# Kernel optimization log

Measured on AMD Instinct MI355X. Metric: run time of the kernel, lower is better.

## Reference

```python
import jax, jax.numpy as jnp
import numpy as np
from functools import partial


def advect(f, vx, vy):
    """Semi-Lagrangian advection with bilinear interpolation and periodic wrap.
    Faithful to the torch version, including its xy-indexed meshgrid."""
    rows, cols = f.shape
    # torch.meshgrid(arange(rows), arange(cols), indexing='xy') == np.meshgrid semantics
    cell_ys, cell_xs = jnp.meshgrid(jnp.arange(rows), jnp.arange(cols), indexing='xy')
    center_xs = (cell_xs - vx).ravel()
    center_ys = (cell_ys - vy).ravel()
    left_ix = jnp.floor(center_xs).astype(jnp.int32)
    top_ix = jnp.floor(center_ys).astype(jnp.int32)
    rw = center_xs - left_ix  # right weight
    bw = center_ys - top_ix   # bottom weight
    left_ix = jnp.mod(left_ix, rows)
    right_ix = jnp.mod(left_ix + 1, rows)
    top_ix = jnp.mod(top_ix, cols)
    bot_ix = jnp.mod(top_ix + 1, cols)
    flat_f = ((1 - rw) * ((1 - bw) * f[left_ix, top_ix] + bw * f[left_ix, bot_ix])
              + rw * ((1 - bw) * f[right_ix, top_ix] + bw * f[right_ix, bot_ix]))
    return flat_f.reshape(rows, cols)


def project(vx, vy):
    """Approximate pressure projection: 10 Jacobi iterations of a 5-point stencil."""
    h = 1.0 / vx.shape[0]
    div = -0.5 * h * (jnp.roll(vx, -1, axis=0) - jnp.roll(vx, 1, axis=0)
                      + jnp.roll(vy, -1, axis=1) - jnp.roll(vy, 1, axis=1))

    def jacobi(k, p):
        return (div + jnp.roll(p, 1, axis=0) + jnp.roll(p, -1, axis=0)
                + jnp.roll(p, 1, axis=1) + jnp.roll(p, -1, axis=1)) / 4.0

    p = jax.lax.fori_loop(0, 10, jacobi, jnp.zeros_like(vx))
    vx = vx - 0.5 * (jnp.roll(p, -1, axis=0) - jnp.roll(p, 1, axis=0)) / h
    vy = vy - 0.5 * (jnp.roll(p, -1, axis=1) - jnp.roll(p, 1, axis=1)) / h
    return vx, vy


def simulate(vx, vy, smoke, num_time_steps):
    def step(carry, _):
        vx, vy, smoke = carry
        vx_upd = advect(vx, vx, vy)
        vy_upd = advect(vy, vx, vy)
        vx, vy = project(vx_upd, vy_upd)
        smoke = advect(smoke, vx, vy)
        return (vx, vy, smoke), None

    (vx, vy, smoke), _ = jax.lax.scan(step, (vx, vy, smoke), None, length=num_time_steps)
    return smoke


def setup_inputs() -> dict:
    key = jax.random.key(0)
    k1, k2, k3 = jax.random.split(key, 3)
    N = 2048
    smoke = jax.random.uniform(k1, (N, N), dtype=jnp.float32)
    init_vx = jax.random.normal(k2, (N, N), dtype=jnp.float32)
    init_vy = jax.random.normal(k3, (N, N), dtype=jnp.float32)
    return {"smoke": smoke, "init_vx": init_vx, "init_vy": init_vy,
            "num_time_steps": 20}


def reference(smoke, init_vx, init_vy, num_time_steps):
    return simulate(init_vx, init_vy, smoke, num_time_steps)
```

## Files before the change

### kernel.cpp

```cpp
#include <hip/hip_runtime.h>

namespace {

constexpr int N = 2048;
constexpr int MASK = N - 1;
constexpr int SH = 11;
constexpr float H = 1.0f / (float)N;

using f32x2 = __attribute__((ext_vector_type(2))) float;


__device__ __forceinline__ float dpp_left(float x) {
  return __int_as_float(__builtin_amdgcn_update_dpp(
      0, __float_as_int(x), 0x111 , 0xF, 0xF, true));
}
__device__ __forceinline__ float dpp_right(float x) {
  return __int_as_float(__builtin_amdgcn_update_dpp(
      0, __float_as_int(x), 0x101 , 0xF, 0xF, true));
}

__global__ __launch_bounds__(256) void advect_vel_k(
    const float* __restrict__ vx, const float* __restrict__ vy,
    float2* __restrict__ OV) {
  int bid = blockIdx.x;
  int sb = ((bid & 7) << 11) | (bid >> 3);
  int idx = sb * 256 + threadIdx.x;
  int i = idx >> SH, j = idx & MASK;
  float cx = (float)i - vx[idx];
  float cy = (float)j - vy[idx];
  float fx = floorf(cx), fy = floorf(cy);
  float rw = cx - fx, bw = cy - fy;
  int l = ((int)fx) & MASK;
  int t = ((int)fy) & MASK;
  int r = (l + 1) & MASK;
  int b = (t + 1) & MASK;
  int i00 = (l << SH) | t, i01 = (l << SH) | b;
  int i10 = (r << SH) | t, i11 = (r << SH) | b;
  float omr = 1.0f - rw, omb = 1.0f - bw;
  float w00 = omr * omb, w01 = omr * bw, w10 = rw * omb, w11 = rw * bw;
  float2 o;
  o.x = w00 * vx[i00] + w01 * vx[i01] + w10 * vx[i10] + w11 * vx[i11];
  o.y = w00 * vy[i00] + w01 * vy[i01] + w10 * vy[i10] + w11 * vy[i11];
  OV[idx] = o;
}

__global__ __launch_bounds__(256) void advect_all_k(
    const float* __restrict__ f,
    const float2* __restrict__ V,
    float* __restrict__ of, float2* __restrict__ OV) {
  int bid = blockIdx.x;
  int sb = ((bid & 7) << 10) | (bid >> 3);
  int t0 = sb * 256 + threadIdx.x;
  int j  = t0 & MASK;
  int i0 = (t0 >> SH) * 2;
  int idx0 = (i0 << SH) | j;
  int idx1 = idx0 + N;

  float2 v0 = V[idx0];
  float2 v1 = V[idx1];

  float cx0 = (float)i0 - v0.x, cy0 = (float)j - v0.y;
  float fx0 = floorf(cx0), fy0 = floorf(cy0);
  float rw0 = cx0 - fx0, bw0 = cy0 - fy0;
  int l0 = ((int)fx0) & MASK, tt0 = ((int)fy0) & MASK;
  int r0 = (l0 + 1) & MASK,  b0 = (tt0 + 1) & MASK;
  int a00 = (l0 << SH) | tt0, a01 = (l0 << SH) | b0;
  int a10 = (r0 << SH) | tt0, a11 = (r0 << SH) | b0;

  float cx1 = (float)(i0 + 1) - v1.x, cy1 = (float)j - v1.y;
  float fx1 = floorf(cx1), fy1 = floorf(cy1);
  float rw1 = cx1 - fx1, bw1 = cy1 - fy1;
  int l1 = ((int)fx1) & MASK, tt1 = ((int)fy1) & MASK;
  int r1 = (l1 + 1) & MASK,  b1 = (tt1 + 1) & MASK;
  int c00 = (l1 << SH) | tt1, c01 = (l1 << SH) | b1;
  int c10 = (r1 << SH) | tt1, c11 = (r1 << SH) | b1;

  float2 g00a = V[a00], g01a = V[a01], g10a = V[a10], g11a = V[a11];
  float  f00a = f[a00], f01a = f[a01], f10a = f[a10], f11a = f[a11];
  float2 g00c = V[c00], g01c = V[c01], g10c = V[c10], g11c = V[c11];
  float  f00c = f[c00], f01c = f[c01], f10c = f[c10], f11c = f[c11];

  float omr0 = 1.0f - rw0, omb0 = 1.0f - bw0;
  float w00a = omr0 * omb0, w01a = omr0 * bw0, w10a = rw0 * omb0, w11a = rw0 * bw0;
  float omr1 = 1.0f - rw1, omb1 = 1.0f - bw1;
  float w00c = omr1 * omb1, w01c = omr1 * bw1, w10c = rw1 * omb1, w11c = rw1 * bw1;

  of[idx0] = w00a * f00a + w01a * f01a + w10a * f10a + w11a * f11a;
  float2 o0;
  o0.x = w00a * g00a.x + w01a * g01a.x + w10a * g10a.x + w11a * g11a.x;
  o0.y = w00a * g00a.y + w01a * g01a.y + w10a * g10a.y + w11a * g11a.y;
  OV[idx0] = o0;
  of[idx1] = w00c * f00c + w01c * f01c + w10c * f10c + w11c * f11c;
  float2 o1;
  o1.x = w00c * g00c.x + w01c * g01c.x + w10c * g10c.x + w11c * g11c.x;
  o1.y = w00c * g00c.y + w01c * g01c.y + w10c * g10c.y + w11c * g11c.y;
  OV[idx1] = o1;
}

__global__ __launch_bounds__(256) void advect_smoke_k(
    const float* __restrict__ f,
    const float2* __restrict__ V,
    float* __restrict__ of) {
  int bid = blockIdx.x;
  int sb = ((bid & 7) << 11) | (bid >> 3);
  int idx = sb * 256 + threadIdx.x;
  int i = idx >> SH, j = idx & MASK;
  float2 v = V[idx];
  float cx = (float)i - v.x;
  float cy = (float)j - v.y;
  float fx = floorf(cx), fy = floorf(cy);
  float rw = cx - fx, bw = cy - fy;
  int l = ((int)fx) & MASK;
  int t = ((int)fy) & MASK;
  int r = (l + 1) & MASK;
  int b = (t + 1) & MASK;
  float f00 = f[(l << SH) | t];
  float f01 = f[(l << SH) | b];
  float f10 = f[(r << SH) | t];
  float f11 = f[(r << SH) | b];
  float omr = 1.0f - rw, omb = 1.0f - bw;
  of[idx] = omr * (omb * f00 + bw * f01) + rw * (omb * f10 + bw * f11);
}

__device__ __forceinline__ float4 jac_row(float4 dd, float4 vu, float4 vd, float4 o) {
  float pl = dpp_left(o.w);
  float pr = dpp_right(o.x);
  f32x2 dlo = {dd.x, dd.y}, dhi = {dd.z, dd.w};
  f32x2 vulo = {vu.x, vu.y}, vuhi = {vu.z, vu.w};
  f32x2 vdlo = {vd.x, vd.y}, vdhi = {vd.z, vd.w};
  f32x2 lft = {pl, o.x};
  f32x2 mid = {o.y, o.z};
  f32x2 rgt = {o.w, pr};
  f32x2 lo = (dlo + vulo + vdlo + lft + mid) * 0.25f;
  f32x2 hi = (dhi + vuhi + vdhi + mid + rgt) * 0.25f;
  return float4{lo.x, lo.y, hi.x, hi.y};
}

__device__ __forceinline__ void div_p1(float4 au, float4 ad, float4 b,
                                       float4& dq, float4& pq) {
  float yl = dpp_left(b.w);
  float yr = dpp_right(b.x);
  constexpr float s = -0.5f * H;
  f32x2 vlo = f32x2{ad.x, ad.y} - f32x2{au.x, au.y};
  f32x2 vhi = f32x2{ad.z, ad.w} - f32x2{au.z, au.w};
  f32x2 hlo = f32x2{b.y, b.z} - f32x2{yl, b.x};
  f32x2 hhi = f32x2{b.w, yr} - f32x2{b.y, b.z};
  f32x2 dlo = (vlo + hlo) * s;
  f32x2 dhi = (vhi + hhi) * s;
  f32x2 plo = dlo * 0.25f;
  f32x2 phi = dhi * 0.25f;
  dq = float4{dlo.x, dlo.y, dhi.x, dhi.y};
  pq = float4{plo.x, plo.y, phi.x, phi.y};
}

__global__ __launch_bounds__(512, 6) void project_k(
    const float2* __restrict__ V,
    float2* __restrict__ OV) {
  __shared__ __align__(16) float pA[90 * 64];
  __shared__ __align__(16) float pB[90 * 64];

  const int tid = threadIdx.x;
  const int bid = blockIdx.x;
  const int sbid = ((bid & 7) << 8) | (bid >> 3);
  const int tile_i = sbid >> 6;
  const int tile_j = sbid & 63;
  const int bi = tile_i * 64 - 11;
  const int cj0 = tile_j * 32 - 16;

  for (int e = tid; e < 86 * 32; e += 512) {
    int row = e >> 5;
    int u = e & 31;
    int gi = (bi + row) & MASK;
    int gj = (cj0 + u * 2) & MASK;
    int gg = (gi << SH) | gj;
    float4 q = *(const float4*)&V[gg];
    *(float2*)&pA[(row + 1) * 64 + u * 2] = float2{q.x, q.z};
    *(float2*)&pB[(row + 1) * 64 + u * 2] = float2{q.y, q.w};
  }
  __syncthreads();

  const int g = tid >> 4;
  const int c0 = (tid & 15) * 4;
  const bool act = (g < 29);
  const int r0 = 3 * g;
  float4 p[3], d[3];
#pragma unroll
  for (int q = 0; q < 3; ++q) { p[q] = float4{0,0,0,0}; d[q] = float4{0,0,0,0}; }

  if (act) {
    const int lb = r0 * 64 + c0;
    float4 a0 = *(const float4*)&pA[lb];
    float4 a1 = *(const float4*)&pA[lb + 64];
    float4 a2 = *(const float4*)&pA[lb + 128];
    float4 a3 = *(const float4*)&pA[lb + 192];
    float4 a4 = *(const float4*)&pA[lb + 256];
    float4 b0 = *(const float4*)&pB[lb + 64];
    float4 b1 = *(const float4*)&pB[lb + 128];
    float4 b2 = *(const float4*)&pB[lb + 192];
    div_p1(a0, a2, b0, d[0], p[0]);
    div_p1(a1, a3, b1, d[1], p[1]);
    div_p1(a2, a4, b2, d[2], p[2]);
  }
  __syncthreads();

#pragma unroll
  for (int k = 0; k < 9; ++k) {
    float* w = (k & 1) ? pB : pA;
    if (act) {
      *(float4*)&w[(r0 + 1) * 64 + c0] = p[0];
      *(float4*)&w[(r0 + 3) * 64 + c0] = p[2];
    }
    __syncthreads();
    if (act) {
      float4 up = *(const float4*)&w[(r0 + 0) * 64 + c0];
      float4 dn = *(const float4*)&w[(r0 + 4) * 64 + c0];
      float4 o0 = p[0], o1 = p[1];
      p[0] = jac_row(d[0], up, o1, o0);
      p[1] = jac_row(d[1], o0, p[2], o1);
      p[2] = jac_row(d[2], o1, dn, p[2]);
    }
  }

  if (act) {
    *(float4*)&pB[(r0 + 1) * 64 + c0] = p[0];
    *(float4*)&pB[(r0 + 2) * 64 + c0] = p[1];
    *(float4*)&pB[(r0 + 3) * 64 + c0] = p[2];
  }
  __syncthreads();

  const float c = 0.5f / H;
#pragma unroll
  for (int q = 0; q < 4; ++q) {
    int pth = tid + q * 512;
    int oi = pth >> 5, oj = pth & 31;
    int gi = tile_i * 64 + oi;
    int gj = tile_j * 32 + oj;
    int gg = (gi << SH) | gj;
    float2 vc = V[gg];
    float2 o;
    o.x = vc.x - c * (pB[(13 + oi) * 64 + 16 + oj] - pB[(11 + oi) * 64 + 16 + oj]);
    o.y = vc.y - c * (pB[(12 + oi) * 64 + 17 + oj] - pB[(12 + oi) * 64 + 15 + oj]);
    OV[gg] = o;
  }
}

}

extern "C" void kernel_launch(void* const* d_in, const int* in_sizes, int n_in,
                              void* d_out, int out_size, void* d_ws, size_t ws_size,
                              hipStream_t stream) {
  const float* smoke_in = (const float*)d_in[0];
  const float* vx_in    = (const float*)d_in[1];
  const float* vy_in    = (const float*)d_in[2];
  float* out = (float*)d_out;

  const size_t fsz = (size_t)N * N;
  float* base = (float*)d_ws;
  float2* VC = (float2*)base;
  float2* VA = (float2*)(base + 2 * fsz);
  float*  SA = base + 4 * fsz;

  dim3 ablk(256), agrd((N * N) / 256);
  dim3 a2grd((N * N) / 512);
  dim3 pblk(512), pgrd(32 * 64);
  const int steps = 20;

  const float* ssrc = smoke_in;

  advect_vel_k<<<agrd, ablk, 0, stream>>>(vx_in, vy_in, VC);

  for (int t = 0; t < steps; ++t) {
    project_k<<<pgrd, pblk, 0, stream>>>(VC, VA);
    float* sdst = (t & 1) ? out : SA;
    if (t < steps - 1) {
      advect_all_k<<<a2grd, ablk, 0, stream>>>(ssrc, VA, sdst, VC);
    } else {
      advect_smoke_k<<<agrd, ablk, 0, stream>>>(ssrc, VA, sdst);
    }
    ssrc = sdst;
  }
}
```

Measured before the change: 1.017 ms.

## Pack velocity and smoke into interleaved float4 so gathers use one load

```diff
diff --git a/kernel.cpp b/kernel.cpp
--- a/kernel.cpp
+++ b/kernel.cpp
@@ -44,10 +44,20 @@
   OV[idx] = o;
 }
 
-__global__ __launch_bounds__(256) void advect_all_k(
-    const float* __restrict__ f,
-    const float2* __restrict__ V,
-    float* __restrict__ of, float2* __restrict__ OV) {
+__global__ __launch_bounds__(256) void pack_smoke_k(
+    const float* __restrict__ f, float* __restrict__ Pf) {
+  int t = blockIdx.x * 256 + threadIdx.x;
+  float4 s = *(const float4*)&f[t * 4];
+  Pf[(t * 4 + 0) * 4 + 2] = s.x;
+  Pf[(t * 4 + 1) * 4 + 2] = s.y;
+  Pf[(t * 4 + 2) * 4 + 2] = s.z;
+  Pf[(t * 4 + 3) * 4 + 2] = s.w;
+}
+
+__global__ __launch_bounds__(256) void advect_packed_k(
+    const float4* __restrict__ P,
+    float* __restrict__ Pn,
+    float2* __restrict__ V2) {
   int bid = blockIdx.x;
   int sb = ((bid & 7) << 10) | (bid >> 3);
   int t0 = sb * 256 + threadIdx.x;
@@ -56,8 +66,9 @@
   int idx0 = (i0 << SH) | j;
   int idx1 = idx0 + N;
 
-  float2 v0 = V[idx0];
-  float2 v1 = V[idx1];
+  const float* Pf = (const float*)P;
+  float2 v0 = *(const float2*)&Pf[idx0 * 4];
+  float2 v1 = *(const float2*)&Pf[idx1 * 4];
 
   float cx0 = (float)i0 - v0.x, cy0 = (float)j - v0.y;
   float fx0 = floorf(cx0), fy0 = floorf(cy0);
@@ -75,16 +86,100 @@
   int c00 = (l1 << SH) | tt1, c01 = (l1 << SH) | b1;
   int c10 = (r1 << SH) | tt1, c11 = (r1 << SH) | b1;
 
+  float4 g00a = P[a00], g01a = P[a01], g10a = P[a10], g11a = P[a11];
+  float4 g00c = P[c00], g01c = P[c01], g10c = P[c10], g11c = P[c11];
+
+  float omr0 = 1.0f - rw0, omb0 = 1.0f - bw0;
+  float w00a = omr0 * omb0, w01a = omr0 * bw0, w10a = rw0 * omb0, w11a = rw0 * bw0;
+  float omr1 = 1.0f - rw1, omb1 = 1.0f - bw1;
+  float w00c = omr1 * omb1, w01c = omr1 * bw1, w10c = rw1 * omb1, w11c = rw1 * bw1;
+
+  float2 o0, o1;
+  o0.x = w00a * g00a.x + w01a * g01a.x + w10a * g10a.x + w11a * g11a.x;
+  o0.y = w00a * g00a.y + w01a * g01a.y + w10a * g10a.y + w11a * g11a.y;
+  float sm0 = w00a * g00a.z + w01a * g01a.z + w10a * g10a.z + w11a * g11a.z;
+  o1.x = w00c * g00c.x + w01c * g01c.x + w10c * g10c.x + w11c * g11c.x;
+  o1.y = w00c * g00c.y + w01c * g01c.y + w10c * g10c.y + w11c * g11c.y;
+  float sm1 = w00c * g00c.z + w01c * g01c.z + w10c * g10c.z + w11c * g11c.z;
+
+  V2[idx0] = o0;
+  V2[idx1] = o1;
+  Pn[idx0 * 4 + 2] = sm0;
+  Pn[idx1 * 4 + 2] = sm1;
+}
+
+__global__ __launch_bounds__(256) void advect_last_k(
+    const float4* __restrict__ P,
+    float* __restrict__ of) {
+  int bid = blockIdx.x;
+  int sb = ((bid & 7) << 10) | (bid >> 3);
+  int t0 = sb * 256 + threadIdx.x;
+  int j  = t0 & MASK;
+  int i0 = (t0 >> SH) * 2;
+  int idx0 = (i0 << SH) | j;
+  int idx1 = idx0 + N;
+
+  const float* Pf = (const float*)P;
+  float2 v0 = *(const float2*)&Pf[idx0 * 4];
+  float2 v1 = *(const float2*)&Pf[idx1 * 4];
+
+  float cx0 = (float)i0 - v0.x, cy0 = (float)j - v0.y;
+  float fx0 = floorf(cx0), fy0 = floorf(cy0);
+  float rw0 = cx0 - fx0, bw0 = cy0 - fy0;
+  int l0 = ((int)fx0) & MASK, tt0 = ((int)fy0) & MASK;
+  int r0 = (l0 + 1) & MASK,  b0 = (tt0 + 1) & MASK;
+  float4 g00a = P[(l0 << SH) | tt0], g01a = P[(l0 << SH) | b0];
+  float4 g10a = P[(r0 << SH) | tt0], g11a = P[(r0 << SH) | b0];
+
+  float cx1 = (float)(i0 + 1) - v1.x, cy1 = (float)j - v1.y;
+  float fx1 = floorf(cx1), fy1 = floorf(cy1);
+  float rw1 = cx1 - fx1, bw1 = cy1 - fy1;
+  int l1 = ((int)fx1) & MASK, tt1 = ((int)fy1) & MASK;
+  int r1 = (l1 + 1) & MASK,  b1 = (tt1 + 1) & MASK;
+  float4 g00c = P[(l1 << SH) | tt1], g01c = P[(l1 << SH) | b1];
+  float4 g10c = P[(r1 << SH) | tt1], g11c = P[(r1 << SH) | b1];
+
+  float omr0 = 1.0f - rw0, omb0 = 1.0f - bw0;
+  float omr1 = 1.0f - rw1, omb1 = 1.0f - bw1;
+  of[idx0] = omr0 * (omb0 * g00a.z + bw0 * g01a.z) + rw0 * (omb0 * g10a.z + bw0 * g11a.z);
+  of[idx1] = omr1 * (omb1 * g00c.z + bw1 * g01c.z) + rw1 * (omb1 * g10c.z + bw1 * g11c.z);
+}
+
+__global__ __launch_bounds__(256) void advect_all_k(
+    const float* __restrict__ f,
+    const float2* __restrict__ V,
+    float* __restrict__ of, float2* __restrict__ OV) {
+  int bid = blockIdx.x;
+  int sb = ((bid & 7) << 10) | (bid >> 3);
+  int t0 = sb * 256 + threadIdx.x;
+  int j  = t0 & MASK;
+  int i0 = (t0 >> SH) * 2;
+  int idx0 = (i0 << SH) | j;
+  int idx1 = idx0 + N;
+  float2 v0 = V[idx0];
+  float2 v1 = V[idx1];
+  float cx0 = (float)i0 - v0.x, cy0 = (float)j - v0.y;
+  float fx0 = floorf(cx0), fy0 = floorf(cy0);
+  float rw0 = cx0 - fx0, bw0 = cy0 - fy0;
+  int l0 = ((int)fx0) & MASK, tt0 = ((int)fy0) & MASK;
+  int r0 = (l0 + 1) & MASK,  b0 = (tt0 + 1) & MASK;
+  int a00 = (l0 << SH) | tt0, a01 = (l0 << SH) | b0;
+  int a10 = (r0 << SH) | tt0, a11 = (r0 << SH) | b0;
+  float cx1 = (float)(i0 + 1) - v1.x, cy1 = (float)j - v1.y;
+  float fx1 = floorf(cx1), fy1 = floorf(cy1);
+  float rw1 = cx1 - fx1, bw1 = cy1 - fy1;
+  int l1 = ((int)fx1) & MASK, tt1 = ((int)fy1) & MASK;
+  int r1 = (l1 + 1) & MASK,  b1 = (tt1 + 1) & MASK;
+  int c00 = (l1 << SH) | tt1, c01 = (l1 << SH) | b1;
+  int c10 = (r1 << SH) | tt1, c11 = (r1 << SH) | b1;
   float2 g00a = V[a00], g01a = V[a01], g10a = V[a10], g11a = V[a11];
   float  f00a = f[a00], f01a = f[a01], f10a = f[a10], f11a = f[a11];
   float2 g00c = V[c00], g01c = V[c01], g10c = V[c10], g11c = V[c11];
   float  f00c = f[c00], f01c = f[c01], f10c = f[c10], f11c = f[c11];
-
   float omr0 = 1.0f - rw0, omb0 = 1.0f - bw0;
   float w00a = omr0 * omb0, w01a = omr0 * bw0, w10a = rw0 * omb0, w11a = rw0 * bw0;
   float omr1 = 1.0f - rw1, omb1 = 1.0f - bw1;
   float w00c = omr1 * omb1, w01c = omr1 * bw1, w10c = rw1 * omb1, w11c = rw1 * bw1;
-
   of[idx0] = w00a * f00a + w01a * f01a + w10a * f10a + w11a * f11a;
   float2 o0;
   o0.x = w00a * g00a.x + w01a * g01a.x + w10a * g10a.x + w11a * g11a.x;
@@ -153,9 +248,10 @@
   pq = float4{plo.x, plo.y, phi.x, phi.y};
 }
 
+template <int OSTR>
 __global__ __launch_bounds__(512, 6) void project_k(
     const float2* __restrict__ V,
-    float2* __restrict__ OV) {
+    float* __restrict__ OVf) {
   __shared__ __align__(16) float pA[90 * 64];
   __shared__ __align__(16) float pB[90 * 64];
 
@@ -240,7 +336,7 @@
     float2 o;
     o.x = vc.x - c * (pB[(13 + oi) * 64 + 16 + oj] - pB[(11 + oi) * 64 + 16 + oj]);
     o.y = vc.y - c * (pB[(12 + oi) * 64 + 17 + oj] - pB[(12 + oi) * 64 + 15 + oj]);
-    OV[gg] = o;
+    *(float2*)&OVf[(size_t)gg * OSTR] = o;
   }
 }
 
@@ -256,27 +352,46 @@
 
   const size_t fsz = (size_t)N * N;
   float* base = (float*)d_ws;
-  float2* VC = (float2*)base;
-  float2* VA = (float2*)(base + 2 * fsz);
-  float*  SA = base + 4 * fsz;
 
   dim3 ablk(256), agrd((N * N) / 256);
   dim3 a2grd((N * N) / 512);
   dim3 pblk(512), pgrd(32 * 64);
   const int steps = 20;
 
-  const float* ssrc = smoke_in;
-
-  advect_vel_k<<<agrd, ablk, 0, stream>>>(vx_in, vy_in, VC);
-
-  for (int t = 0; t < steps; ++t) {
-    project_k<<<pgrd, pblk, 0, stream>>>(VC, VA);
-    float* sdst = (t & 1) ? out : SA;
-    if (t < steps - 1) {
-      advect_all_k<<<a2grd, ablk, 0, stream>>>(ssrc, VA, sdst, VC);
-    } else {
-      advect_smoke_k<<<agrd, ablk, 0, stream>>>(ssrc, VA, sdst);
+  const size_t need = fsz * 10 * sizeof(float);
+
+  if (ws_size >= need) {
+    float4* P0 = (float4*)base;
+    float4* P1 = (float4*)(base + 4 * fsz);
+    float2* V2 = (float2*)(base + 8 * fsz);
+
+    advect_vel_k<<<agrd, ablk, 0, stream>>>(vx_in, vy_in, V2);
+    pack_smoke_k<<<(N * N) / 1024, ablk, 0, stream>>>(smoke_in, (float*)P0);
+
+    for (int t = 0; t < steps; ++t) {
+      float4* Pc = (t & 1) ? P1 : P0;
+      float4* Pn = (t & 1) ? P0 : P1;
+      project_k<4><<<pgrd, pblk, 0, stream>>>(V2, (float*)Pc);
+      if (t < steps - 1)
+        advect_packed_k<<<a2grd, ablk, 0, stream>>>(Pc, (float*)Pn, V2);
+      else
+        advect_last_k<<<a2grd, ablk, 0, stream>>>(Pc, out);
     }
-    ssrc = sdst;
-  }
-}
+  } else {
+    float2* VC = (float2*)base;
+    float2* VA = (float2*)(base + 2 * fsz);
+    float*  SA = base + 4 * fsz;
+
+    const float* ssrc = smoke_in;
+    advect_vel_k<<<agrd, ablk, 0, stream>>>(vx_in, vy_in, VC);
+    for (int t = 0; t < steps; ++t) {
+      project_k<2><<<pgrd, pblk, 0, stream>>>(VC, (float*)VA);
+      float* sdst = (t & 1) ? out : SA;
+      if (t < steps - 1)
+        advect_all_k<<<a2grd, ablk, 0, stream>>>(ssrc, VA, sdst, VC);
+      else
+        advect_smoke_k<<<agrd, ablk, 0, stream>>>(ssrc, VA, sdst);
+      ssrc = sdst;
+    }
+  }
+}
```

Result: slower. 1.295 ms (+27.4%).

## Pack velocity and smoke into float4 array for single-gather advection

Applied to the files above, without the earlier changes.

```diff
diff --git a/kernel.cpp b/kernel.cpp
--- a/kernel.cpp
+++ b/kernel.cpp
@@ -44,10 +44,10 @@
   OV[idx] = o;
 }
 
-__global__ __launch_bounds__(256) void advect_all_k(
-    const float* __restrict__ f,
-    const float2* __restrict__ V,
-    float* __restrict__ of, float2* __restrict__ OV) {
+__global__ __launch_bounds__(256) void advect_packed_k(
+    const float4* __restrict__ P,
+    float* __restrict__ Sn,
+    float2* __restrict__ V2) {
   int bid = blockIdx.x;
   int sb = ((bid & 7) << 10) | (bid >> 3);
   int t0 = sb * 256 + threadIdx.x;
@@ -56,8 +56,9 @@
   int idx0 = (i0 << SH) | j;
   int idx1 = idx0 + N;
 
-  float2 v0 = V[idx0];
-  float2 v1 = V[idx1];
+  const float* Pf = (const float*)P;
+  float2 v0 = *(const float2*)&Pf[idx0 * 4];
+  float2 v1 = *(const float2*)&Pf[idx1 * 4];
 
   float cx0 = (float)i0 - v0.x, cy0 = (float)j - v0.y;
   float fx0 = floorf(cx0), fy0 = floorf(cy0);
@@ -75,51 +76,63 @@
   int c00 = (l1 << SH) | tt1, c01 = (l1 << SH) | b1;
   int c10 = (r1 << SH) | tt1, c11 = (r1 << SH) | b1;
 
-  float2 g00a = V[a00], g01a = V[a01], g10a = V[a10], g11a = V[a11];
-  float  f00a = f[a00], f01a = f[a01], f10a = f[a10], f11a = f[a11];
-  float2 g00c = V[c00], g01c = V[c01], g10c = V[c10], g11c = V[c11];
-  float  f00c = f[c00], f01c = f[c01], f10c = f[c10], f11c = f[c11];
+  float4 g00a = P[a00], g01a = P[a01], g10a = P[a10], g11a = P[a11];
+  float4 g00c = P[c00], g01c = P[c01], g10c = P[c10], g11c = P[c11];
 
   float omr0 = 1.0f - rw0, omb0 = 1.0f - bw0;
   float w00a = omr0 * omb0, w01a = omr0 * bw0, w10a = rw0 * omb0, w11a = rw0 * bw0;
   float omr1 = 1.0f - rw1, omb1 = 1.0f - bw1;
   float w00c = omr1 * omb1, w01c = omr1 * bw1, w10c = rw1 * omb1, w11c = rw1 * bw1;
 
-  of[idx0] = w00a * f00a + w01a * f01a + w10a * f10a + w11a * f11a;
-  float2 o0;
+  float2 o0, o1;
   o0.x = w00a * g00a.x + w01a * g01a.x + w10a * g10a.x + w11a * g11a.x;
   o0.y = w00a * g00a.y + w01a * g01a.y + w10a * g10a.y + w11a * g11a.y;
-  OV[idx0] = o0;
-  of[idx1] = w00c * f00c + w01c * f01c + w10c * f10c + w11c * f11c;
-  float2 o1;
+  float sm0 = w00a * g00a.z + w01a * g01a.z + w10a * g10a.z + w11a * g11a.z;
   o1.x = w00c * g00c.x + w01c * g01c.x + w10c * g10c.x + w11c * g11c.x;
   o1.y = w00c * g00c.y + w01c * g01c.y + w10c * g10c.y + w11c * g11c.y;
-  OV[idx1] = o1;
-}
-
-__global__ __launch_bounds__(256) void advect_smoke_k(
-    const float* __restrict__ f,
-    const float2* __restrict__ V,
+  float sm1 = w00c * g00c.z + w01c * g01c.z + w10c * g10c.z + w11c * g11c.z;
+
+  V2[idx0] = o0;
+  V2[idx1] = o1;
+  Sn[idx0] = sm0;
+  Sn[idx1] = sm1;
+}
+
+__global__ __launch_bounds__(256) void advect_last_k(
+    const float4* __restrict__ P,
     float* __restrict__ of) {
   int bid = blockIdx.x;
-  int sb = ((bid & 7) << 11) | (bid >> 3);
-  int idx = sb * 256 + threadIdx.x;
-  int i = idx >> SH, j = idx & MASK;
-  float2 v = V[idx];
-  float cx = (float)i - v.x;
-  float cy = (float)j - v.y;
-  float fx = floorf(cx), fy = floorf(cy);
-  float rw = cx - fx, bw = cy - fy;
-  int l = ((int)fx) & MASK;
-  int t = ((int)fy) & MASK;
-  int r = (l + 1) & MASK;
-  int b = (t + 1) & MASK;
-  float f00 = f[(l << SH) | t];
-  float f01 = f[(l << SH) | b];
-  float f10 = f[(r << SH) | t];
-  float f11 = f[(r << SH) | b];
-  float omr = 1.0f - rw, omb = 1.0f - bw;
-  of[idx] = omr * (omb * f00 + bw * f01) + rw * (omb * f10 + bw * f11);
+  int sb = ((bid & 7) << 10) | (bid >> 3);
+  int t0 = sb * 256 + threadIdx.x;
+  int j  = t0 & MASK;
+  int i0 = (t0 >> SH) * 2;
+  int idx0 = (i0 << SH) | j;
+  int idx1 = idx0 + N;
+
+  const float* Pf = (const float*)P;
+  float2 v0 = *(const float2*)&Pf[idx0 * 4];
+  float2 v1 = *(const float2*)&Pf[idx1 * 4];
+
+  float cx0 = (float)i0 - v0.x, cy0 = (float)j - v0.y;
+  float fx0 = floorf(cx0), fy0 = floorf(cy0);
+  float rw0 = cx0 - fx0, bw0 = cy0 - fy0;
+  int l0 = ((int)fx0) & MASK, tt0 = ((int)fy0) & MASK;
+  int r0 = (l0 + 1) & MASK,  b0 = (tt0 + 1) & MASK;
+  float4 g00a = P[(l0 << SH) | tt0], g01a = P[(l0 << SH) | b0];
+  float4 g10a = P[(r0 << SH) | tt0], g11a = P[(r0 << SH) | b0];
+
+  float cx1 = (float)(i0 + 1) - v1.x, cy1 = (float)j - v1.y;
+  float fx1 = floorf(cx1), fy1 = floorf(cy1);
+  float rw1 = cx1 - fx1, bw1 = cy1 - fy1;
+  int l1 = ((int)fx1) & MASK, tt1 = ((int)fy1) & MASK;
+  int r1 = (l1 + 1) & MASK,  b1 = (tt1 + 1) & MASK;
+  float4 g00c = P[(l1 << SH) | tt1], g01c = P[(l1 << SH) | b1];
+  float4 g10c = P[(r1 << SH) | tt1], g11c = P[(r1 << SH) | b1];
+
+  float omr0 = 1.0f - rw0, omb0 = 1.0f - bw0;
+  float omr1 = 1.0f - rw1, omb1 = 1.0f - bw1;
+  of[idx0] = omr0 * (omb0 * g00a.z + bw0 * g01a.z) + rw0 * (omb0 * g10a.z + bw0 * g11a.z);
+  of[idx1] = omr1 * (omb1 * g00c.z + bw1 * g01c.z) + rw1 * (omb1 * g10c.z + bw1 * g11c.z);
 }
 
 __device__ __forceinline__ float4 jac_row(float4 dd, float4 vu, float4 vd, float4 o) {
@@ -155,7 +168,8 @@
 
 __global__ __launch_bounds__(512, 6) void project_k(
     const float2* __restrict__ V,
-    float2* __restrict__ OV) {
+    const float* __restrict__ S,
+    float4* __restrict__ P) {
   __shared__ __align__(16) float pA[90 * 64];
   __shared__ __align__(16) float pB[90 * 64];
 
@@ -237,10 +251,13 @@
     int gj = tile_j * 32 + oj;
     int gg = (gi << SH) | gj;
     float2 vc = V[gg];
-    float2 o;
+    float sm = S[gg];
+    float4 o;
     o.x = vc.x - c * (pB[(13 + oi) * 64 + 16 + oj] - pB[(11 + oi) * 64 + 16 + oj]);
     o.y = vc.y - c * (pB[(12 + oi) * 64 + 17 + oj] - pB[(12 + oi) * 64 + 15 + oj]);
-    OV[gg] = o;
+    o.z = sm;
+    o.w = 0.0f;
+    P[gg] = o;
   }
 }
 
@@ -256,27 +273,25 @@
 
   const size_t fsz = (size_t)N * N;
   float* base = (float*)d_ws;
-  float2* VC = (float2*)base;
-  float2* VA = (float2*)(base + 2 * fsz);
-  float*  SA = base + 4 * fsz;
+  float4* P  = (float4*)base;
+  float*  S  = base + 4 * fsz;
+  float2* VC = (float2*)(base + 5 * fsz);
 
   dim3 ablk(256), agrd((N * N) / 256);
   dim3 a2grd((N * N) / 512);
   dim3 pblk(512), pgrd(32 * 64);
   const int steps = 20;
 
-  const float* ssrc = smoke_in;
-
   advect_vel_k<<<agrd, ablk, 0, stream>>>(vx_in, vy_in, VC);
 
+  const float* scur = smoke_in;
   for (int t = 0; t < steps; ++t) {
-    project_k<<<pgrd, pblk, 0, stream>>>(VC, VA);
-    float* sdst = (t & 1) ? out : SA;
+    project_k<<<pgrd, pblk, 0, stream>>>(VC, scur, P);
     if (t < steps - 1) {
-      advect_all_k<<<a2grd, ablk, 0, stream>>>(ssrc, VA, sdst, VC);
+      advect_packed_k<<<a2grd, ablk, 0, stream>>>(P, S, VC);
+      scur = S;
     } else {
-      advect_smoke_k<<<agrd, ablk, 0, stream>>>(ssrc, VA, sdst);
+      advect_last_k<<<a2grd, ablk, 0, stream>>>(P, out);
     }
-    ssrc = sdst;
-  }
-}
+  }
+}
```

Measured after the change: 1.061 ms. 4.4% more time.
